# Kernel optimization log

Measured on AMD Instinct MI355X. Metric: run time of the kernel, lower is better.

## Reference

```python
import jax, jax.numpy as jnp
import numpy as np

EPS = 1e-5

def conv1d(x, w, b, pad):
    # x: (B,Cin,T), w: (Cout,Cin,K)
    y = jax.lax.conv_general_dilated(x, w, (1,), [(pad, pad)],
                                     dimension_numbers=('NCW', 'OIW', 'NCW'))
    return y + b[None, :, None]

def group_norm(x, scale, bias, groups):
    B, C, T = x.shape
    xg = x.reshape(B, groups, C // groups, T)
    mu = xg.mean(axis=(2, 3), keepdims=True)
    var = xg.var(axis=(2, 3), keepdims=True)
    xn = ((xg - mu) * jax.lax.rsqrt(var + EPS)).reshape(B, C, T)
    return xn * scale[None, :, None] + bias[None, :, None]

def setup_inputs() -> dict:
    key = jax.random.key(0)
    ks = jax.random.split(key, 16)
    T, B = 1024, 128
    class_size, style_size, char_style_size = 80, 256, 64
    hidden, n_out = 128, 1
    cin = class_size + style_size + char_style_size  # 400
    def w(k, shape, fan_in):
        return jax.random.normal(k, shape, jnp.float32) * (1.0 / np.sqrt(fan_in))
    inp = {
        'input': jax.random.normal(ks[0], (T, B, class_size), jnp.float32),
        'g_style': jax.random.normal(ks[1], (B, style_size), jnp.float32),
        'spacing_style': jax.random.normal(ks[2], (B, 8), jnp.float32),
        'char_style': jax.random.normal(ks[3], (B, class_size, char_style_size), jnp.float32),
        'conv1_w': w(ks[4], (hidden, cin, 3), cin * 3),
        'conv1_b': jnp.zeros((hidden,), jnp.float32),
        'gn1_s': jnp.ones((hidden,), jnp.float32),
        'gn1_b': jnp.zeros((hidden,), jnp.float32),
        'conv2_w': w(ks[5], (hidden // 2, hidden, 3), hidden * 3),
        'conv2_b': jnp.zeros((hidden // 2,), jnp.float32),
        'gn2_s': jnp.ones((hidden // 2,), jnp.float32),
        'gn2_b': jnp.zeros((hidden // 2,), jnp.float32),
        'conv3_w': w(ks[6], (hidden // 4, hidden // 2, 3), (hidden // 2) * 3),
        'conv3_b': jnp.zeros((hidden // 4,), jnp.float32),
        'gn3_s': jnp.ones((hidden // 4,), jnp.float32),
        'gn3_b': jnp.zeros((hidden // 4,), jnp.float32),
        'conv4_w': w(ks[7], (n_out, hidden // 4, 1), hidden // 4),
        'conv4_b': jnp.zeros((n_out,), jnp.float32),
        'mean': jnp.full((1, n_out), 2.0, jnp.float32),
        'std': jnp.full((1, n_out), 1.0, jnp.float32),
    }
    return inp

def reference(input, g_style, spacing_style, char_style,
              conv1_w, conv1_b, gn1_s, gn1_b,
              conv2_w, conv2_b, gn2_s, gn2_b,
              conv3_w, conv3_b, gn3_s, gn3_b,
              conv4_w, conv4_b, mean, std):
    T, B, _ = input.shape
    # vectorized char-style gather (replaces the python double loop)
    text_chars = jnp.argmax(input, axis=2)                      # (T,B)
    input_style = char_style[jnp.arange(B)[None, :], text_chars]  # (T,B,Dc)
    gs = jnp.broadcast_to(g_style[None], (T,) + g_style.shape)    # (T,B,Ds)
    x = jnp.concatenate([input, gs, input_style], axis=2)         # (T,B,Cin)
    x = x.transpose(1, 2, 0)                                      # (B,Cin,T)
    x = jax.nn.relu(group_norm(conv1d(x, conv1_w, conv1_b, 1), gn1_s, gn1_b, 32))
    x = jax.nn.relu(group_norm(conv1d(x, conv2_w, conv2_b, 1), gn2_s, gn2_b, 32))
    x = jax.nn.relu(group_norm(conv1d(x, conv3_w, conv3_b, 1), gn3_s, gn3_b, 32))
    x = conv1d(x, conv4_w, conv4_b, 0)                            # (B,n_out,T)
    out = x.transpose(2, 0, 1)                                    # (T,B,n_out)
    return out * std + mean
```

## Files before the change

kernel.cpp:

```cpp
#include <hip/hip_runtime.h>
#include <hip/hip_bf16.h>

#define T_LEN 1024
#define BATCH 128
#define NM 131072

typedef __attribute__((ext_vector_type(8))) short short8;
typedef __attribute__((ext_vector_type(4))) float f32x4;

__device__ __forceinline__ float b2f(ushort u) {
  union { uint i; float f; } c; c.i = ((uint)u) << 16; return c.f;
}
__device__ __forceinline__ ushort f2b(float f) {
  __hip_bfloat16 h = __float2bfloat16(f);
  return *reinterpret_cast<ushort*>(&h);
}
__device__ __forceinline__ uint pack2(float a, float b) {
  return (uint)f2b(a) | ((uint)f2b(b) << 16);
}

__global__ __launch_bounds__(256) void k_prep(const float* __restrict__ inp,
    const float* __restrict__ gsty,
    const float* __restrict__ w1, const float* __restrict__ b1,
    const float* __restrict__ w2, const float* __restrict__ w3,
    int* __restrict__ idx, float* __restrict__ Gfull, float* __restrict__ Gk0, float* __restrict__ Gk2,
    ushort* __restrict__ Wp1, ushort* __restrict__ Wp2, ushort* __restrict__ Wp3) {
  int bid = blockIdx.x, tid = threadIdx.x;
  if (bid < 1024) {
    int b0 = (bid >> 5) * 4;
    int t0 = (bid & 31) * 32;
    int q = tid & 3;
    int u = tid >> 2;
    int bp = u & 3;
    int tpA = u >> 2, tpB = tpA + 16;
    int mA = (t0 + tpA)*128 + b0 + bp;
    int mB = (t0 + tpB)*128 + b0 + bp;
    const float* rpA = inp + (size_t)mA*80 + q*20;
    const float* rpB = inp + (size_t)mB*80 + q*20;
    float va[20], vb[20];
    #pragma unroll
    for (int i = 0; i < 5; ++i) {
      float4 ua = *(const float4*)(rpA + i*4);
      va[i*4+0]=ua.x; va[i*4+1]=ua.y; va[i*4+2]=ua.z; va[i*4+3]=ua.w;
    }
    #pragma unroll
    for (int i = 0; i < 5; ++i) {
      float4 ub = *(const float4*)(rpB + i*4);
      vb[i*4+0]=ub.x; vb[i*4+1]=ub.y; vb[i*4+2]=ub.z; vb[i*4+3]=ub.w;
    }
    {
      float best = va[0]; int bi = q*20;
      #pragma unroll
      for (int i = 1; i < 20; ++i) if (va[i] > best) { best = va[i]; bi = q*20 + i; }
      #pragma unroll
      for (int d = 1; d <= 2; d <<= 1) {
        float ob = __shfl_xor(best, d);
        int   oi = __shfl_xor(bi, d);
        if (ob > best || (ob == best && oi < bi)) { best = ob; bi = oi; }
      }
      if (q == 0) idx[mA] = bi;
    }
    {
      float best = vb[0]; int bi = q*20;
      #pragma unroll
      for (int i = 1; i < 20; ++i) if (vb[i] > best) { best = vb[i]; bi = q*20 + i; }
      #pragma unroll
      for (int d = 1; d <= 2; d <<= 1) {
        float ob = __shfl_xor(best, d);
        int   oi = __shfl_xor(bi, d);
        if (ob > best || (ob == best && oi < bi)) { best = ob; bi = oi; }
      }
      if (q == 0) idx[mB] = bi;
    }
  } else if (bid < 1152) {
    int b = bid - 1024;
    __shared__ float gl[256];
    gl[tid] = gsty[b*256 + tid];
    __syncthreads();
    if (tid < 128) {
      int o = tid;
      const float* wr = w1 + (size_t)o*1200 + 240;
      float s0 = 0.f, s1 = 0.f, s2 = 0.f;
      for (int c = 0; c < 256; ++c) {
        float g = gl[c];
        s0 += wr[c*3+0]*g; s1 += wr[c*3+1]*g; s2 += wr[c*3+2]*g;
      }
      Gk0[b*128+o] = s0;
      Gk2[b*128+o] = s2;
      Gfull[b*128+o] = s0 + s1 + s2 + b1[o];
    }
  } else {
    int e = (bid - 1152)*256 + tid;
    if (e < 61440) {
      int o = e / 480, r = e % 480, k = r / 160, c = r % 160;
      float v = 0.f;
      if (c < 80)       v = w1[(size_t)o*1200 + c*3 + k];
      else if (c >= 96) v = w1[(size_t)o*1200 + (336 + (c-96))*3 + k];
      Wp1[e] = f2b(v);
    } else if (e < 61440 + 24576) {
      int e2 = e - 61440;
      int o = e2/384, r = e2%384, k = r/128, c = r%128;
      Wp2[e2] = f2b(w2[(size_t)o*384 + c*3 + k]);
    } else if (e < 61440 + 24576 + 6144) {
      int e3 = e - 61440 - 24576;
      int o = e3/192, r = e3%192, k = r/64, c = r%64;
      Wp3[e3] = f2b(w3[(size_t)o*192 + c*3 + k]);
    }
  }
}

__device__ __forceinline__ void c1_ldg(const float* __restrict__ inp, const float* __restrict__ cs,
                                       const int* idxs, int b, int cc, int t0, int task,
                                       float4& fa, float4& fb) {
  int r = task >> 2, q = task & 3;
  int t = t0 - 1 + r;
  fa = make_float4(0.f,0.f,0.f,0.f); fb = fa;
  if (t >= 0 && t < T_LEN) {
    const float* src;
    if (cc < 3) {
      int c8 = cc*32 + q*8;
      if (c8 >= 80) return;
      src = inp + ((size_t)t*BATCH + b)*80 + c8;
    } else {
      int jc = idxs[r];
      src = cs + ((size_t)b*80 + jc)*64 + (cc-3)*32 + q*8;
    }
    fa = *(const float4*)src;
    fb = *(const float4*)(src + 4);
  }
}
__device__ __forceinline__ uint4 packf(float4 a, float4 b) {
  uint4 p;
  p.x = pack2(a.x, a.y); p.y = pack2(a.z, a.w);
  p.z = pack2(b.x, b.y); p.w = pack2(b.z, b.w);
  return p;
}
__device__ __forceinline__ short8 c1_ldw(const ushort* Wp1, int cc, int task) {
  int o = task / 12, seg = task % 12;
  int k = seg >> 2, oct = seg & 3;
  return *(const short8*)(Wp1 + (size_t)o*480 + k*160 + cc*32 + oct*8);
}
__device__ __forceinline__ void c1_wrx(ushort (*Xsb)[40], int task, uint4 v) {
  int r = task >> 2, q = task & 3;
  *(uint4*)&Xsb[r][q*8] = v;
}
__device__ __forceinline__ void c1_wrw(ushort (*Wsb)[104], int task, short8 v) {
  int o = task / 12, seg = task % 12;
  *(short8*)&Wsb[o][seg*8] = v;
}

__global__ __launch_bounds__(256) void k_conv1(const float* __restrict__ inp, const float* __restrict__ cs,
    const int* __restrict__ idx, const ushort* __restrict__ Wp1,
    const float* __restrict__ Gfull, const float* __restrict__ Gk0, const float* __restrict__ Gk2,
    ushort* __restrict__ y1, float2* __restrict__ part1) {
  __shared__ __align__(16) ushort Xs[2][130][40];
  __shared__ __align__(16) ushort Ws[2][128][104];
  __shared__ float gf[128], g0v[128], g2v[128];
  __shared__ float ps[4][128], pq[4][128];
  __shared__ int idxs[130];
  int b = blockIdx.x, tt = blockIdx.y;
  int t0 = tt * 128;
  int tid = threadIdx.x, lane = tid & 63, wave = tid >> 6;
  int ln = lane & 15, lq = lane >> 4, wt = wave * 32;

  if (tid < 130) {
    int t = t0 - 1 + tid;
    idxs[tid] = (t >= 0 && t < T_LEN) ? idx[t*BATCH + b] : 0;
  }
  if (tid < 128) {
    gf[tid]  = Gfull[b*128 + tid];
    g0v[tid] = Gk0[b*128 + tid];
    g2v[tid] = Gk2[b*128 + tid];
  }
  f32x4 acc[2][8];
  #pragma unroll
  for (int m = 0; m < 2; ++m)
    #pragma unroll
    for (int n = 0; n < 8; ++n) { f32x4 z = {0.f,0.f,0.f,0.f}; acc[m][n] = z; }

  float4 fa0, fb0, fa1, fb1, fa2, fb2;
  short8 rw[6];

  c1_ldg(inp, cs, idxs, b, 0, t0, tid, fa0, fb0);
  c1_ldg(inp, cs, idxs, b, 0, t0, tid + 256, fa1, fb1);
  if (tid < 8) c1_ldg(inp, cs, idxs, b, 0, t0, tid + 512, fa2, fb2);
  #pragma unroll
  for (int i = 0; i < 6; ++i) rw[i] = c1_ldw(Wp1, 0, tid + i*256);
  c1_wrx(Xs[0], tid, packf(fa0, fb0));
  c1_wrx(Xs[0], tid + 256, packf(fa1, fb1));
  if (tid < 8) c1_wrx(Xs[0], tid + 512, packf(fa2, fb2));
  #pragma unroll
  for (int i = 0; i < 6; ++i) c1_wrw(Ws[0], tid + i*256, rw[i]);
  __syncthreads();

  for (int cc = 0; cc < 5; ++cc) {
    bool more = (cc < 4);
    if (more) {
      c1_ldg(inp, cs, idxs, b, cc+1, t0, tid, fa0, fb0);
      c1_ldg(inp, cs, idxs, b, cc+1, t0, tid + 256, fa1, fb1);
      if (tid < 8) c1_ldg(inp, cs, idxs, b, cc+1, t0, tid + 512, fa2, fb2);
      #pragma unroll
      for (int i = 0; i < 6; ++i) rw[i] = c1_ldw(Wp1, cc+1, tid + i*256);
    }
    int cur = cc & 1;
    #pragma unroll
    for (int k = 0; k < 3; ++k) {
      short8 a0 = *(const short8*)&Xs[cur][wt + ln + k][lq*8];
      short8 a1 = *(const short8*)&Xs[cur][wt + 16 + ln + k][lq*8];
      #pragma unroll
      for (int nt = 0; nt < 8; ++nt) {
        short8 bb = *(const short8*)&Ws[cur][nt*16 + ln][k*32 + lq*8];
        acc[0][nt] = __builtin_amdgcn_mfma_f32_16x16x32_bf16(a0, bb, acc[0][nt], 0, 0, 0);
        acc[1][nt] = __builtin_amdgcn_mfma_f32_16x16x32_bf16(a1, bb, acc[1][nt], 0, 0, 0);
      }
    }
    if (more) {
      int nxt = cur ^ 1;
      c1_wrx(Xs[nxt], tid, packf(fa0, fb0));
      c1_wrx(Xs[nxt], tid + 256, packf(fa1, fb1));
      if (tid < 8) c1_wrx(Xs[nxt], tid + 512, packf(fa2, fb2));
      #pragma unroll
      for (int i = 0; i < 6; ++i) c1_wrw(Ws[nxt], tid + i*256, rw[i]);
    }
    __syncthreads();
  }

  #pragma unroll
  for (int nt = 0; nt < 8; ++nt) {
    int o = nt*16 + ln;
    float add = gf[o];
    float s = 0.f, sq = 0.f;
    #pragma unroll
    for (int mt = 0; mt < 2; ++mt) {
      int tb = t0 + wt + mt*16 + lq*4;
      float vv[4];
      #pragma unroll
      for (int r = 0; r < 4; ++r) {
        float v = acc[mt][nt][r] + add;
        int t = tb + r;
        if (t == 0) v -= g0v[o];
        if (t == T_LEN-1) v -= g2v[o];
        vv[r] = v; s += v; sq += v*v;
      }
      uint2 pk;
      pk.x = pack2(vv[0], vv[1]);
      pk.y = pack2(vv[2], vv[3]);
      *(uint2*)(y1 + ((size_t)b*128 + o)*T_LEN + tb) = pk;
    }
    s  += __shfl_xor(s, 16);  s  += __shfl_xor(s, 32);
    sq += __shfl_xor(sq, 16); sq += __shfl_xor(sq, 32);
    if (lane < 16) { ps[wave][o] = s; pq[wave][o] = sq; }
  }
  __syncthreads();
  if (tid < 128) {
    float S = ps[0][tid]+ps[1][tid]+ps[2][tid]+ps[3][tid];
    float Q = pq[0][tid]+pq[1][tid]+pq[2][tid]+pq[3][tid];
    part1[((size_t)b*128 + tid)*8 + tt] = make_float2(S, Q);
  }
}

__device__ __forceinline__ short8 mid_ldw(const ushort* Wp, int cin, int cc, int task) {
  int o = task / 12, seg = task % 12;
  int k = seg >> 2, oct = seg & 3;
  return *(const short8*)(Wp + ((size_t)o*3 + k)*cin + cc*32 + oct*8);
}
__device__ __forceinline__ void mid_wrw(ushort (*Wsb)[104], int task, short8 v) {
  int o = task / 12, seg = task % 12;
  *(short8*)&Wsb[o][seg*8] = v;
}

template<int NC, int CO, int NT, int CPG>
__global__ __launch_bounds__(256) void k_convmid(const ushort* __restrict__ xin,
    const ushort* __restrict__ Wp, const float* __restrict__ bias,
    const float2* __restrict__ partin, const float* __restrict__ gs, const float* __restrict__ gb,
    ushort* __restrict__ yout, float2* __restrict__ part) {
  constexpr int CIN = NC*32;
  constexpr int NG = CIN/CPG;
  __shared__ __align__(16) ushort Xs[2][130][40];
  __shared__ __align__(16) ushort Ws[2][CO][104];
  __shared__ float2 affl[CIN];
  __shared__ float ssb[CIN], qqb[CIN];
  __shared__ float2 gmr[NG];
  __shared__ float bl[CO];
  __shared__ float ps[4][CO], pq[4][CO];
  int b = blockIdx.x, tt = blockIdx.y, t0 = tt*128;
  int tid = threadIdx.x, lane = tid & 63, wave = tid >> 6;
  int ln = lane & 15, lq = lane >> 4, wt = wave*32;
  int cp = (tid & 15)*2, j = tid >> 4;
  int er = (tid < 32) ? 0 : 129, eci = tid & 31;
  const ushort* xb = xin + (size_t)b * CIN * T_LEN;

  if (tid < CIN) {
    const float2* p = partin + (size_t)(b*CIN + tid)*8;
    float S = 0.f, Q = 0.f;
    #pragma unroll
    for (int j2 = 0; j2 < 8; ++j2) { float2 v = p[j2]; S += v.x; Q += v.y; }
    ssb[tid] = S; qqb[tid] = Q;
  }
  if (tid < CO)  bl[tid]  = bias[tid];

  f32x4 acc[2][NT];
  #pragma unroll
  for (int m = 0; m < 2; ++m)
    #pragma unroll
    for (int n = 0; n < NT; ++n) { f32x4 z = {0.f,0.f,0.f,0.f}; acc[m][n] = z; }

  short8 v0, v1;
  ushort ev = 0;
  short8 rw0, rw1, rw2;
  int te = t0 - 1 + er;

  {
    const ushort* s0 = xb + (size_t)cp * T_LEN + t0 + j*8;
    v0 = *(const short8*)s0;
    v1 = *(const short8*)(s0 + T_LEN);
    ev = 0;
    if (tid < 64 && te >= 0 && te < T_LEN) ev = xb[(size_t)eci * T_LEN + te];
    rw0 = mid_ldw(Wp, CIN, 0, tid);
    if constexpr (CO == 64) {
      rw1 = mid_ldw(Wp, CIN, 0, tid + 256);
      rw2 = mid_ldw(Wp, CIN, 0, tid + 512);
    } else {
      if (tid < 128) rw1 = mid_ldw(Wp, CIN, 0, tid + 256);
    }
  }
  __syncthreads();
  if (tid < NG) {
    float S = 0.f, Q = 0.f;
    #pragma unroll
    for (int ci = 0; ci < CPG; ++ci) { S += ssb[tid*CPG+ci]; Q += qqb[tid*CPG+ci]; }
    float invn = 1.f / (float)(CPG * T_LEN);
    float m = S * invn;
    float var = Q * invn - m*m;
    gmr[tid] = make_float2(m, rsqrtf(var + 1e-5f));
  }
  __syncthreads();
  if (tid < CIN) {
    float2 mr = gmr[tid / CPG];
    float a = mr.y * gs[tid];
    affl[tid] = make_float2(a, gb[tid] - mr.x * a);
  }
  __syncthreads();
  {
    float2 A0 = affl[cp], A1 = affl[cp+1];
    #pragma unroll
    for (int e = 0; e < 8; ++e) {
      float f0 = fmaxf(0.f, b2f((ushort)v0[e])*A0.x + A0.y);
      float f1 = fmaxf(0.f, b2f((ushort)v1[e])*A1.x + A1.y);
      *(uint*)&Xs[0][1 + j*8 + e][cp] = pack2(f0, f1);
    }
    if (tid < 64) {
      ushort val = 0;
      if (te >= 0 && te < T_LEN) { float2 A = affl[eci]; val = f2b(fmaxf(0.f, b2f(ev)*A.x + A.y)); }
      Xs[0][er][eci] = val;
    }
    mid_wrw(Ws[0], tid, rw0);
    if constexpr (CO == 64) {
      mid_wrw(Ws[0], tid + 256, rw1);
      mid_wrw(Ws[0], tid + 512, rw2);
    } else {
      if (tid < 128) mid_wrw(Ws[0], tid + 256, rw1);
    }
  }
  __syncthreads();

  for (int cc = 0; cc < NC; ++cc) {
    bool more = (cc + 1 < NC);
    if (more) {
      const ushort* s0 = xb + (size_t)((cc+1)*32 + cp) * T_LEN + t0 + j*8;
      v0 = *(const short8*)s0;
      v1 = *(const short8*)(s0 + T_LEN);
      ev = 0;
      if (tid < 64 && te >= 0 && te < T_LEN) ev = xb[(size_t)((cc+1)*32 + eci) * T_LEN + te];
      rw0 = mid_ldw(Wp, CIN, cc+1, tid);
      if constexpr (CO == 64) {
        rw1 = mid_ldw(Wp, CIN, cc+1, tid + 256);
        rw2 = mid_ldw(Wp, CIN, cc+1, tid + 512);
      } else {
        if (tid < 128) rw1 = mid_ldw(Wp, CIN, cc+1, tid + 256);
      }
    }
    int cur = cc & 1;
    #pragma unroll
    for (int k = 0; k < 3; ++k) {
      short8 a0 = *(const short8*)&Xs[cur][wt + ln + k][lq*8];
      short8 a1 = *(const short8*)&Xs[cur][wt + 16 + ln + k][lq*8];
      #pragma unroll
      for (int nt = 0; nt < NT; ++nt) {
        short8 bb = *(const short8*)&Ws[cur][nt*16 + ln][k*32 + lq*8];
        acc[0][nt] = __builtin_amdgcn_mfma_f32_16x16x32_bf16(a0, bb, acc[0][nt], 0, 0, 0);
        acc[1][nt] = __builtin_amdgcn_mfma_f32_16x16x32_bf16(a1, bb, acc[1][nt], 0, 0, 0);
      }
    }
    if (more) {
      int nxt = cur ^ 1;
      float2 A0 = affl[(cc+1)*32 + cp], A1 = affl[(cc+1)*32 + cp + 1];
      #pragma unroll
      for (int e = 0; e < 8; ++e) {
        float f0 = fmaxf(0.f, b2f((ushort)v0[e])*A0.x + A0.y);
        float f1 = fmaxf(0.f, b2f((ushort)v1[e])*A1.x + A1.y);
        *(uint*)&Xs[nxt][1 + j*8 + e][cp] = pack2(f0, f1);
      }
      if (tid < 64) {
        ushort val = 0;
        if (te >= 0 && te < T_LEN) { float2 A = affl[(cc+1)*32 + eci]; val = f2b(fmaxf(0.f, b2f(ev)*A.x + A.y)); }
        Xs[nxt][er][eci] = val;
      }
      mid_wrw(Ws[nxt], tid, rw0);
      if constexpr (CO == 64) {
        mid_wrw(Ws[nxt], tid + 256, rw1);
        mid_wrw(Ws[nxt], tid + 512, rw2);
      } else {
        if (tid < 128) mid_wrw(Ws[nxt], tid + 256, rw1);
      }
    }
    __syncthreads();
  }

  #pragma unroll
  for (int nt = 0; nt < NT; ++nt) {
    int o = nt*16 + ln;
    float add = bl[o];
    float s = 0.f, sq = 0.f;
    #pragma unroll
    for (int mt = 0; mt < 2; ++mt) {
      int tb = t0 + wt + mt*16 + lq*4;
      float vv[4];
      #pragma unroll
      for (int r = 0; r < 4; ++r) {
        float v = acc[mt][nt][r] + add;
        vv[r] = v; s += v; sq += v*v;
      }
      uint2 pk;
      pk.x = pack2(vv[0], vv[1]);
      pk.y = pack2(vv[2], vv[3]);
      *(uint2*)(yout + ((size_t)b*CO + o)*T_LEN + tb) = pk;
    }
    s  += __shfl_xor(s, 16);  s  += __shfl_xor(s, 32);
    sq += __shfl_xor(sq, 16); sq += __shfl_xor(sq, 32);
    if (lane < 16) { ps[wave][o] = s; pq[wave][o] = sq; }
  }
  __syncthreads();
  if (tid < CO) {
    float S = ps[0][tid]+ps[1][tid]+ps[2][tid]+ps[3][tid];
    float Q = pq[0][tid]+pq[1][tid]+pq[2][tid]+pq[3][tid];
    part[((size_t)b*CO + tid)*8 + tt] = make_float2(S, Q);
  }
}

__global__ __launch_bounds__(256) void k_final(const ushort* __restrict__ y3, const float2* __restrict__ part3,
    const float* __restrict__ s3, const float* __restrict__ b3,
    const float* __restrict__ w4, const float* __restrict__ b4,
    const float* __restrict__ mn, const float* __restrict__ sd, float* __restrict__ out) {
  int b = blockIdx.x;
  int t = blockIdx.y * 256 + threadIdx.x;
  __shared__ float wl[32];
  __shared__ float2 al[32];
  if (threadIdx.x < 32) {
    int c = threadIdx.x;
    const float2* p = part3 + (size_t)(b*32 + c)*8;
    float S = 0.f, Q = 0.f;
    #pragma unroll
    for (int j = 0; j < 8; ++j) { float2 v = p[j]; S += v.x; Q += v.y; }
    float invn = 1.f / (float)T_LEN;
    float m = S * invn;
    float var = Q * invn - m*m;
    float rs = rsqrtf(var + 1e-5f);
    float a = rs * s3[c];
    al[c] = make_float2(a, b3[c] - m*a);
    wl[c] = w4[c];
  }
  __syncthreads();
  float s = b4[0];
  #pragma unroll 8
  for (int c = 0; c < 32; ++c) {
    float v = b2f(y3[((size_t)b*32 + c)*T_LEN + t]);
    float2 A = al[c];
    s += wl[c] * fmaxf(0.f, v*A.x + A.y);
  }
  out[(size_t)t*BATCH + b] = s*sd[0] + mn[0];
}

extern "C" void kernel_launch(void* const* d_in, const int* in_sizes, int n_in,
                              void* d_out, int out_size, void* d_ws, size_t ws_size,
                              hipStream_t stream) {
  const float* inp  = (const float*)d_in[0];
  const float* gsty = (const float*)d_in[1];
  const float* cs   = (const float*)d_in[3];
  const float* w1   = (const float*)d_in[4];
  const float* b1   = (const float*)d_in[5];
  const float* gn1s = (const float*)d_in[6];
  const float* gn1b = (const float*)d_in[7];
  const float* w2   = (const float*)d_in[8];
  const float* b2   = (const float*)d_in[9];
  const float* gn2s = (const float*)d_in[10];
  const float* gn2b = (const float*)d_in[11];
  const float* w3   = (const float*)d_in[12];
  const float* b3   = (const float*)d_in[13];
  const float* gn3s = (const float*)d_in[14];
  const float* gn3b = (const float*)d_in[15];
  const float* w4   = (const float*)d_in[16];
  const float* b4   = (const float*)d_in[17];
  const float* mn   = (const float*)d_in[18];
  const float* sd   = (const float*)d_in[19];
  float* out = (float*)d_out;
  ushort* wsu = (ushort*)d_ws;

  int*    idx = (int*)wsu;
  ushort* Wp1 = wsu + (size_t)262144;
  ushort* Wp2 = Wp1 + 61440;
  ushort* Wp3 = Wp2 + 24576;
  float* Gfull = (float*)(Wp3 + 6144);
  float* Gk0   = Gfull + 16384;
  float* Gk2   = Gk0 + 16384;
  ushort* y1 = (ushort*)(Gk2 + 16384);
  ushort* y2 = y1 + (size_t)NM*128;
  ushort* y3 = y2 + (size_t)NM*64;
  float2* part1 = (float2*)(y3 + (size_t)NM*32);
  float2* part2 = part1 + 131072;
  float2* part3 = part2 + 65536;

  k_prep<<<1512, 256, 0, stream>>>(inp, gsty, w1, b1, w2, w3,
                                   idx, Gfull, Gk0, Gk2, Wp1, Wp2, Wp3);
  k_conv1<<<dim3(128,8), 256, 0, stream>>>(inp, cs, idx, Wp1, Gfull, Gk0, Gk2, y1, part1);
  k_convmid<4,64,4,4><<<dim3(128,8), 256, 0, stream>>>(y1, Wp2, b2, part1, gn1s, gn1b, y2, part2);
  k_convmid<2,32,2,2><<<dim3(128,8), 256, 0, stream>>>(y2, Wp3, b3, part2, gn2s, gn2b, y3, part3);
  k_final<<<dim3(128,4), 256, 0, stream>>>(y3, part3, gn3s, gn3b, w4, b4, mn, sd, out);
}
```

Measured before the change: 94.81 us.

## Fuse argmax character-index computation into conv1 input loading

Removes the argmax section from the prep kernel and computes the per-timestep argmax inside conv1, reusing the class-channel values it already loads for the first chunks. The reduction is finished with cross-lane shuffles and written to shared memory before the char-style chunks (cc>=3) are fetched. This avoids a separate full read of the input tensor and the global idx round-trip. It adds shuffle work and relies on idxs being written and synchronized before the chunk-3 gather, which happens after the loop's later barrier.

```diff
diff --git a/kernel.cpp b/kernel.cpp
--- a/kernel.cpp
+++ b/kernel.cpp
@@ -19,61 +19,14 @@
   return (uint)f2b(a) | ((uint)f2b(b) << 16);
 }
 
-__global__ __launch_bounds__(256) void k_prep(const float* __restrict__ inp,
-    const float* __restrict__ gsty,
+__global__ __launch_bounds__(256) void k_prep(const float* __restrict__ gsty,
     const float* __restrict__ w1, const float* __restrict__ b1,
     const float* __restrict__ w2, const float* __restrict__ w3,
-    int* __restrict__ idx, float* __restrict__ Gfull, float* __restrict__ Gk0, float* __restrict__ Gk2,
+    float* __restrict__ Gfull, float* __restrict__ Gk0, float* __restrict__ Gk2,
     ushort* __restrict__ Wp1, ushort* __restrict__ Wp2, ushort* __restrict__ Wp3) {
   int bid = blockIdx.x, tid = threadIdx.x;
-  if (bid < 1024) {
-    int b0 = (bid >> 5) * 4;
-    int t0 = (bid & 31) * 32;
-    int q = tid & 3;
-    int u = tid >> 2;
-    int bp = u & 3;
-    int tpA = u >> 2, tpB = tpA + 16;
-    int mA = (t0 + tpA)*128 + b0 + bp;
-    int mB = (t0 + tpB)*128 + b0 + bp;
-    const float* rpA = inp + (size_t)mA*80 + q*20;
-    const float* rpB = inp + (size_t)mB*80 + q*20;
-    float va[20], vb[20];
-    #pragma unroll
-    for (int i = 0; i < 5; ++i) {
-      float4 ua = *(const float4*)(rpA + i*4);
-      va[i*4+0]=ua.x; va[i*4+1]=ua.y; va[i*4+2]=ua.z; va[i*4+3]=ua.w;
-    }
-    #pragma unroll
-    for (int i = 0; i < 5; ++i) {
-      float4 ub = *(const float4*)(rpB + i*4);
-      vb[i*4+0]=ub.x; vb[i*4+1]=ub.y; vb[i*4+2]=ub.z; vb[i*4+3]=ub.w;
-    }
-    {
-      float best = va[0]; int bi = q*20;
-      #pragma unroll
-      for (int i = 1; i < 20; ++i) if (va[i] > best) { best = va[i]; bi = q*20 + i; }
-      #pragma unroll
-      for (int d = 1; d <= 2; d <<= 1) {
-        float ob = __shfl_xor(best, d);
-        int   oi = __shfl_xor(bi, d);
-        if (ob > best || (ob == best && oi < bi)) { best = ob; bi = oi; }
-      }
-      if (q == 0) idx[mA] = bi;
-    }
-    {
-      float best = vb[0]; int bi = q*20;
-      #pragma unroll
-      for (int i = 1; i < 20; ++i) if (vb[i] > best) { best = vb[i]; bi = q*20 + i; }
-      #pragma unroll
-      for (int d = 1; d <= 2; d <<= 1) {
-        float ob = __shfl_xor(best, d);
-        int   oi = __shfl_xor(bi, d);
-        if (ob > best || (ob == best && oi < bi)) { best = ob; bi = oi; }
-      }
-      if (q == 0) idx[mB] = bi;
-    }
-  } else if (bid < 1152) {
-    int b = bid - 1024;
+  if (bid < 128) {
+    int b = bid;
     __shared__ float gl[256];
     gl[tid] = gsty[b*256 + tid];
     __syncthreads();
@@ -90,7 +43,7 @@
       Gfull[b*128+o] = s0 + s1 + s2 + b1[o];
     }
   } else {
-    int e = (bid - 1152)*256 + tid;
+    int e = (bid - 128)*256 + tid;
     if (e < 61440) {
       int o = e / 480, r = e % 480, k = r / 160, c = r % 160;
       float v = 0.f;
@@ -129,6 +82,13 @@
     fb = *(const float4*)(src + 4);
   }
 }
+__device__ __forceinline__ void amax8(float& best, int& bi, float4 fa, float4 fb, int base, bool valid) {
+  if (!valid) return;
+  float v[8] = {fa.x, fa.y, fa.z, fa.w, fb.x, fb.y, fb.z, fb.w};
+  #pragma unroll
+  for (int i = 0; i < 8; ++i)
+    if (v[i] > best) { best = v[i]; bi = base + i; }
+}
 __device__ __forceinline__ uint4 packf(float4 a, float4 b) {
   uint4 p;
   p.x = pack2(a.x, a.y); p.y = pack2(a.z, a.w);
@@ -150,7 +110,7 @@
 }
 
 __global__ __launch_bounds__(256) void k_conv1(const float* __restrict__ inp, const float* __restrict__ cs,
-    const int* __restrict__ idx, const ushort* __restrict__ Wp1,
+    const ushort* __restrict__ Wp1,
     const float* __restrict__ Gfull, const float* __restrict__ Gk0, const float* __restrict__ Gk2,
     ushort* __restrict__ y1, float2* __restrict__ part1) {
   __shared__ __align__(16) ushort Xs[2][130][40];
@@ -162,11 +122,8 @@
   int t0 = tt * 128;
   int tid = threadIdx.x, lane = tid & 63, wave = tid >> 6;
   int ln = lane & 15, lq = lane >> 4, wt = wave * 32;
-
-  if (tid < 130) {
-    int t = t0 - 1 + tid;
-    idxs[tid] = (t >= 0 && t < T_LEN) ? idx[t*BATCH + b] : 0;
-  }
+  int q = tid & 3, u = tid >> 2;
+
   if (tid < 128) {
     gf[tid]  = Gfull[b*128 + tid];
     g0v[tid] = Gk0[b*128 + tid];
@@ -180,10 +137,15 @@
 
   float4 fa0, fb0, fa1, fb1, fa2, fb2;
   short8 rw[6];
+  float bm0 = -1e30f, bm1 = -1e30f, bm2 = -1e30f;
+  int ib0 = 0, ib1 = 0, ib2 = 0;
 
   c1_ldg(inp, cs, idxs, b, 0, t0, tid, fa0, fb0);
   c1_ldg(inp, cs, idxs, b, 0, t0, tid + 256, fa1, fb1);
   if (tid < 8) c1_ldg(inp, cs, idxs, b, 0, t0, tid + 512, fa2, fb2);
+  amax8(bm0, ib0, fa0, fb0, q*8, true);
+  amax8(bm1, ib1, fa1, fb1, q*8, true);
+  if (tid < 8) amax8(bm2, ib2, fa2, fb2, q*8, true);
   #pragma unroll
   for (int i = 0; i < 6; ++i) rw[i] = c1_ldw(Wp1, 0, tid + i*256);
   c1_wrx(Xs[0], tid, packf(fa0, fb0));
@@ -199,6 +161,27 @@
       c1_ldg(inp, cs, idxs, b, cc+1, t0, tid, fa0, fb0);
       c1_ldg(inp, cs, idxs, b, cc+1, t0, tid + 256, fa1, fb1);
       if (tid < 8) c1_ldg(inp, cs, idxs, b, cc+1, t0, tid + 512, fa2, fb2);
+      if (cc < 2) {
+        int base = (cc+1)*32 + q*8;
+        bool valid = (cc+1 < 2) || (q < 2);
+        amax8(bm0, ib0, fa0, fb0, base, valid);
+        amax8(bm1, ib1, fa1, fb1, base, valid);
+        if (tid < 8) amax8(bm2, ib2, fa2, fb2, base, valid);
+      }
+      if (cc == 1) {
+        #pragma unroll
+        for (int d = 1; d <= 2; d <<= 1) {
+          float ob; int oi;
+          ob = __shfl_xor(bm0, d); oi = __shfl_xor(ib0, d);
+          if (ob > bm0 || (ob == bm0 && oi < ib0)) { bm0 = ob; ib0 = oi; }
+          ob = __shfl_xor(bm1, d); oi = __shfl_xor(ib1, d);
+          if (ob > bm1 || (ob == bm1 && oi < ib1)) { bm1 = ob; ib1 = oi; }
+          ob = __shfl_xor(bm2, d); oi = __shfl_xor(ib2, d);
+          if (ob > bm2 || (ob == bm2 && oi < ib2)) { bm2 = ob; ib2 = oi; }
+        }
+        if (q == 0) { idxs[u] = ib0; idxs[u + 64] = ib1; }
+        if (tid < 8 && (tid & 3) == 0) idxs[128 + (tid >> 2)] = ib2;
+      }
       #pragma unroll
       for (int i = 0; i < 6; ++i) rw[i] = c1_ldw(Wp1, cc+1, tid + i*256);
     }
@@ -506,8 +489,7 @@
   float* out = (float*)d_out;
   ushort* wsu = (ushort*)d_ws;
 
-  int*    idx = (int*)wsu;
-  ushort* Wp1 = wsu + (size_t)262144;
+  ushort* Wp1 = wsu;
   ushort* Wp2 = Wp1 + 61440;
   ushort* Wp3 = Wp2 + 24576;
   float* Gfull = (float*)(Wp3 + 6144);
@@ -520,9 +502,9 @@
   float2* part2 = part1 + 131072;
   float2* part3 = part2 + 65536;
 
-  k_prep<<<1512, 256, 0, stream>>>(inp, gsty, w1, b1, w2, w3,
-                                   idx, Gfull, Gk0, Gk2, Wp1, Wp2, Wp3);
-  k_conv1<<<dim3(128,8), 256, 0, stream>>>(inp, cs, idx, Wp1, Gfull, Gk0, Gk2, y1, part1);
+  k_prep<<<488, 256, 0, stream>>>(gsty, w1, b1, w2, w3,
+                                  Gfull, Gk0, Gk2, Wp1, Wp2, Wp3);
+  k_conv1<<<dim3(128,8), 256, 0, stream>>>(inp, cs, Wp1, Gfull, Gk0, Gk2, y1, part1);
   k_convmid<4,64,4,4><<<dim3(128,8), 256, 0, stream>>>(y1, Wp2, b2, part1, gn1s, gn1b, y2, part2);
   k_convmid<2,32,2,2><<<dim3(128,8), 256, 0, stream>>>(y2, Wp3, b3, part2, gn2s, gn2b, y3, part3);
   k_final<<<dim3(128,4), 256, 0, stream>>>(y3, part3, gn3s, gn3b, w4, b4, mn, sd, out);
```

Result: faster. 89.51 us (-5.6%).
